# Kernel tuning notes

Measured on AMD Instinct MI355X. Metric: run time of the kernel, lower is better.

Reference implementation:

```python
import jax, jax.numpy as jnp
import numpy as np

B, N, C = 8, 2049, 768
H, NB = 12, 4
HD = C // H          # 64
SPB = (N - 1) // NB  # 512
SCALE = HD ** -0.5
EPS = 1e-6


def layer_norm(x, w, b):
    mu = jnp.mean(x, axis=-1, keepdims=True)
    var = jnp.mean((x - mu) ** 2, axis=-1, keepdims=True)
    return (x - mu) * jax.lax.rsqrt(var + EPS) * w + b


def setup_inputs() -> dict:
    key = jax.random.key(0)
    ks = jax.random.split(key, 6)
    s = lambda fan_in: 1.0 / np.sqrt(fan_in)
    return {
        "x": jax.random.normal(ks[0], (B, N, C), jnp.float32),
        "ln1_w": jnp.ones((C,), jnp.float32),
        "ln1_b": jnp.zeros((C,), jnp.float32),
        "qkv_w": jax.random.normal(ks[1], (3 * C, C), jnp.float32) * s(C),
        "proj_w": jax.random.normal(ks[2], (C, C), jnp.float32) * s(C),
        "proj_b": jnp.zeros((C,), jnp.float32),
        "ln2_w": jnp.ones((C,), jnp.float32),
        "ln2_b": jnp.zeros((C,), jnp.float32),
        "fc1_w": jax.random.normal(ks[3], (4 * C, C), jnp.float32) * s(C),
        "fc1_b": jnp.zeros((4 * C,), jnp.float32),
        "fc2_w": jax.random.normal(ks[4], (C, 4 * C), jnp.float32) * s(4 * C),
        "fc2_b": jnp.zeros((C,), jnp.float32),
    }


def _sdpa(q, k, v):
    # q:[...,Q,D] k,v:[...,K,D]
    scores = jnp.einsum("...qd,...kd->...qk", q, k) * SCALE
    return jnp.einsum("...qk,...kd->...qd", jax.nn.softmax(scores, axis=-1), v)


def _attention(h, qkv_w, proj_w, proj_b):
    # h: [B,N,C] (already layer-normed)
    qkv = (h @ qkv_w.T).reshape(B, N, 3, H, HD).transpose(2, 0, 3, 1, 4)  # [3,B,H,N,HD]
    q, k, v = qkv[0], qkv[1], qkv[2]

    # cls token attends globally over all N keys
    cls_att = _sdpa(q[:, :, 0:1, :], k, v)            # [B,H,1,HD]
    cls = cls_att.reshape(B, 1, C) + h[:, 0:1, :]      # benign reshape (seq=1)

    qkv_c = (cls @ qkv_w.T).reshape(B, 1, 3, H, HD).transpose(2, 0, 3, 1, 4)  # [3,B,H,1,HD]
    qc, kc, vc = qkv_c[0], qkv_c[1], qkv_c[2]

    # per-branch local attention with shared cls kv prepended
    def branch(t, tc):
        tb = t[:, :, 1:, :].reshape(B, H, NB, SPB, HD)
        tcb = jnp.broadcast_to(tc[:, :, None, :, :], (B, H, NB, 1, HD))
        return jnp.concatenate([tcb, tb], axis=3)      # [B,H,NB,SPB+1,HD]

    out = _sdpa(branch(q, qc), branch(k, kc), branch(v, vc))[:, :, :, 1:, :]  # [B,H,NB,SPB,HD]
    # faithful replication of the source's reshape((B, spb, C)) on a [B,H,spb,HD]
    # tensor WITHOUT head transpose (raw row-major reinterpretation):
    out = out.transpose(0, 2, 1, 3, 4).reshape(B, NB, SPB, C).reshape(B, NB * SPB, C)

    y = jnp.concatenate([cls, out], axis=1)            # [B,N,C]
    return y @ proj_w.T + proj_b


def reference(x, ln1_w, ln1_b, qkv_w, proj_w, proj_b, ln2_w, ln2_b, fc1_w, fc1_b, fc2_w, fc2_b):
    x = x + _attention(layer_norm(x, ln1_w, ln1_b), qkv_w, proj_w, proj_b)
    h = layer_norm(x, ln2_w, ln2_b)
    h = jax.nn.gelu(h @ fc1_w.T + fc1_b, approximate=False) @ fc2_w.T + fc2_b
    return x + h
```

## Files before the change

### kernel.cpp

```cpp
#include <hip/hip_runtime.h>
#include <hip/hip_bf16.h>

typedef unsigned short u16;
typedef __attribute__((ext_vector_type(8))) short s16x8;
typedef __attribute__((ext_vector_type(4))) float f32x4;

#define MFMA16 __builtin_amdgcn_mfma_f32_16x16x32_bf16
#define AS1 __attribute__((address_space(1)))
#define AS3 __attribute__((address_space(3)))

__device__ __forceinline__ u16 f2bf(float f) {
    union { __hip_bfloat16 h; u16 u; } cv;
    cv.h = __float2bfloat16(f);
    return cv.u;
}
__device__ __forceinline__ float bf2f(u16 u) {
    unsigned int v = ((unsigned int)u) << 16;
    return __uint_as_float(v);
}
__device__ __forceinline__ void gll16(const u16* g, u16* l) {
    __builtin_amdgcn_global_load_lds((AS1 void*)g, (AS3 void*)l, 16, 0, 0);
}

__global__ void cvt_kernel(const float* __restrict__ src, u16* __restrict__ dst, int n) {
    int i = (blockIdx.x * 256 + threadIdx.x) * 4;
    if (i + 3 < n) {
        float4 v = *(const float4*)&src[i];
        u16 o0 = f2bf(v.x), o1 = f2bf(v.y), o2 = f2bf(v.z), o3 = f2bf(v.w);
        ushort4 o; o.x = o0; o.y = o1; o.z = o2; o.w = o3;
        *(ushort4*)&dst[i] = o;
    }
}

__global__ __launch_bounds__(256) void ln_kernel(const float* __restrict__ x,
                                                 const float* __restrict__ w,
                                                 const float* __restrict__ b,
                                                 u16* __restrict__ out) {
    int tok = blockIdx.x;
    int tid = threadIdx.x;
    const float* xr = x + (size_t)tok * 768;
    float v0 = xr[tid], v1 = xr[tid + 256], v2 = xr[tid + 512];
    float s = v0 + v1 + v2;
    float s2 = v0 * v0 + v1 * v1 + v2 * v2;
    #pragma unroll
    for (int d = 1; d < 64; d <<= 1) { s += __shfl_xor(s, d); s2 += __shfl_xor(s2, d); }
    __shared__ float red[8];
    int wv = tid >> 6, l = tid & 63;
    if (l == 0) { red[wv] = s; red[4 + wv] = s2; }
    __syncthreads();
    s = red[0] + red[1] + red[2] + red[3];
    s2 = red[4] + red[5] + red[6] + red[7];
    float mu = s * (1.0f / 768.0f);
    float var = s2 * (1.0f / 768.0f) - mu * mu;
    float rs = rsqrtf(var + 1e-6f);
    u16* orow = out + (size_t)tok * 768;
    orow[tid]       = f2bf((v0 - mu) * rs * w[tid]       + b[tid]);
    orow[tid + 256] = f2bf((v1 - mu) * rs * w[tid + 256] + b[tid + 256]);
    orow[tid + 512] = f2bf((v2 - mu) * rs * w[tid + 512] + b[tid + 512]);
}

template<int EPI>
__global__ __launch_bounds__(256, 2) void gemm_bt(const u16* __restrict__ A,
                                                  const u16* __restrict__ Bw,
                                                  const float* __restrict__ bias,
                                                  const float* __restrict__ res,
                                                  float* __restrict__ outF,
                                                  u16* __restrict__ outU,
                                                  int M, int N, int K) {
    __shared__ u16 lds[8192];
    const int tid = threadIdx.x;
    const int l = tid & 63, w = tid >> 6;
    const int wm = w >> 1, wn = w & 1;
    const int g = l >> 4, c = l & 15;
    const int m0 = blockIdx.y * 128, n0 = blockIdx.x * 128;

    f32x4 zf = {0.f, 0.f, 0.f, 0.f};
    f32x4 acc[4][4];
    #pragma unroll
    for (int m = 0; m < 4; ++m)
        #pragma unroll
        for (int n = 0; n < 4; ++n) acc[m][n] = zf;

    const u16* aS[2]; const u16* bS[2];
    #pragma unroll
    for (int iss = 0; iss < 2; ++iss) {
        int fs = iss * 256 + tid;
        int r = fs >> 2;
        int gk = (fs & 3) ^ ((r >> 1) & 3);
        int ra = m0 + r; if (ra > M - 1) ra = M - 1;
        aS[iss] = A + (size_t)ra * K + gk * 8;
        bS[iss] = Bw + (size_t)(n0 + r) * K + gk * 8;
    }
    u16* aD0 = &lds[(0   + w * 64) * 8];
    u16* aD1 = &lds[(256 + w * 64) * 8];
    u16* bD0 = &lds[4096 + (0   + w * 64) * 8];
    u16* bD1 = &lds[4096 + (256 + w * 64) * 8];

    int aoff[4], boff[4];
    #pragma unroll
    for (int m = 0; m < 4; ++m) {
        int r = wm * 64 + m * 16 + c;
        aoff[m] = r * 32 + ((g ^ ((r >> 1) & 3)) * 8);
        int rb = wn * 64 + m * 16 + c;
        boff[m] = 4096 + rb * 32 + ((g ^ ((rb >> 1) & 3)) * 8);
    }

    for (int k0 = 0; k0 < K; k0 += 32) {
        gll16(aS[0] + k0, aD0);
        gll16(aS[1] + k0, aD1);
        gll16(bS[0] + k0, bD0);
        gll16(bS[1] + k0, bD1);
        __syncthreads();
        s16x8 af[4], bfr[4];
        #pragma unroll
        for (int m = 0; m < 4; ++m) af[m] = *(const s16x8*)&lds[aoff[m]];
        #pragma unroll
        for (int n = 0; n < 4; ++n) bfr[n] = *(const s16x8*)&lds[boff[n]];
        #pragma unroll
        for (int m = 0; m < 4; ++m)
            #pragma unroll
            for (int n = 0; n < 4; ++n)
                acc[m][n] = MFMA16(af[m], bfr[n], acc[m][n], 0, 0, 0);
        __syncthreads();
    }

    #pragma unroll
    for (int n = 0; n < 4; ++n) {
        int col = n0 + wn * 64 + n * 16 + c;
        float bv = (EPI >= 1) ? bias[col] : 0.0f;
        #pragma unroll
        for (int m = 0; m < 4; ++m) {
            int rowb = m0 + wm * 64 + m * 16 + g * 4;
            #pragma unroll
            for (int j = 0; j < 4; ++j) {
                int row = rowb + j;
                if (row < M) {
                    float v = acc[m][n][j];
                    size_t idx = (size_t)row * N + col;
                    if (EPI == 0) {
                        outU[idx] = f2bf(v);
                    } else if (EPI == 1) {
                        outF[idx] = res[idx] + v + bv;
                    } else {
                        float t = v + bv;
                        t = 0.5f * t * (1.0f + erff(t * 0.70710678118654752f));
                        outU[idx] = f2bf(t);
                    }
                }
            }
        }
    }
}

__global__ __launch_bounds__(256) void cls_part(const u16* __restrict__ qkv,
                                                float* __restrict__ part) {
    int bid = blockIdx.x;
    int ch = bid % 17;
    int hh = (bid / 17) % 12;
    int b = bid / (17 * 12);
    int tid = threadIdx.x, l = tid & 63, w = tid >> 6;
    size_t base = (size_t)b * 2049 * 2304;
    float qv = bf2f(qkv[base + hh * 64 + l]);
    __shared__ float sc[128];
    __shared__ float red[8];
    __shared__ float pv[4][64];
    int j0 = ch * 128;
    int nk = 2049 - j0; if (nk > 128) nk = 128;

    for (int jj = w; jj < nk; jj += 4) {
        float kv = bf2f(qkv[base + (size_t)(j0 + jj) * 2304 + 768 + hh * 64 + l]);
        float p = qv * kv;
        p += __shfl_xor(p, 1);  p += __shfl_xor(p, 2);  p += __shfl_xor(p, 4);
        p += __shfl_xor(p, 8);  p += __shfl_xor(p, 16); p += __shfl_xor(p, 32);
        if (l == 0) sc[jj] = p * 0.125f;
    }
    __syncthreads();
    float mx = -1e30f;
    for (int jj = tid; jj < nk; jj += 256) mx = fmaxf(mx, sc[jj]);
    #pragma unroll
    for (int d = 1; d < 64; d <<= 1) mx = fmaxf(mx, __shfl_xor(mx, d));
    if (l == 0) red[w] = mx;
    __syncthreads();
    mx = fmaxf(fmaxf(red[0], red[1]), fmaxf(red[2], red[3]));
    float sum = 0.0f;
    for (int jj = tid; jj < nk; jj += 256) {
        float p = __expf(sc[jj] - mx);
        sc[jj] = p;
        sum += p;
    }
    #pragma unroll
    for (int d = 1; d < 64; d <<= 1) sum += __shfl_xor(sum, d);
    if (l == 0) red[4 + w] = sum;
    __syncthreads();
    sum = red[4] + red[5] + red[6] + red[7];

    float acc = 0.0f;
    for (int jj = w; jj < nk; jj += 4)
        acc += sc[jj] * bf2f(qkv[base + (size_t)(j0 + jj) * 2304 + 1536 + hh * 64 + l]);
    pv[w][l] = acc;
    __syncthreads();
    if (tid < 64) {
        float o = pv[0][tid] + pv[1][tid] + pv[2][tid] + pv[3][tid];
        float* rec = part + ((size_t)(b * 12 + hh) * 17 + ch) * 66;
        rec[2 + tid] = o;
        if (tid == 0) { rec[0] = mx; rec[1] = sum; }
    }
}

__global__ __launch_bounds__(64) void cls_red(const float* __restrict__ part,
                                              const u16* __restrict__ h1,
                                              u16* __restrict__ y) {
    int bid = blockIdx.x;
    int hh = bid % 12, b = bid / 12;
    int l = threadIdx.x;
    const float* recs = part + (size_t)bid * 17 * 66;
    float M = -1e30f;
    #pragma unroll
    for (int i = 0; i < 17; ++i) M = fmaxf(M, recs[i * 66]);
    float den = 0.0f, o = 0.0f;
    #pragma unroll
    for (int i = 0; i < 17; ++i) {
        float scl = __expf(recs[i * 66] - M);
        den += scl * recs[i * 66 + 1];
        o += scl * recs[i * 66 + 2 + l];
    }
    o /= den;
    float r = bf2f(h1[(size_t)b * 2049 * 768 + hh * 64 + l]);
    y[(size_t)b * 1573632 + hh * 64 + l] = f2bf(o + r);
}

__global__ __launch_bounds__(256) void qkvc_gemm(const u16* __restrict__ y,
                                                 const u16* __restrict__ wq,
                                                 u16* __restrict__ qkvc) {
    int tid = threadIdx.x, l = tid & 63, w = tid >> 6;
    int oi = blockIdx.x * 4 + w;
    int b = oi / 2304, n = oi % 2304;
    float acc = 0.0f;
    #pragma unroll
    for (int i = 0; i < 12; ++i) {
        int k = i * 64 + l;
        acc += bf2f(y[(size_t)b * 1573632 + k]) * bf2f(wq[(size_t)n * 768 + k]);
    }
    #pragma unroll
    for (int d = 1; d < 64; d <<= 1) acc += __shfl_xor(acc, d);
    if (l == 0) qkvc[b * 2304 + n] = f2bf(acc);
}

__global__ __launch_bounds__(256, 2) void battn(const u16* __restrict__ qkv,
                                                const u16* __restrict__ qkvc,
                                                u16* __restrict__ y) {
    __shared__ u16 Vt[64 * 40];
    __shared__ u16 Pl[4][32 * 40];
    int bid = blockIdx.x;
    int quarter = bid & 3, nb = (bid >> 2) & 3, h = (bid >> 4) % 12, b = bid / 192;
    int tid = threadIdx.x, l = tid & 63, w = tid >> 6, g = l >> 4, c = l & 15;
    int qbase = quarter * 128 + w * 32;
    size_t tokbase = (size_t)b * 2049 + 1 + (size_t)nb * 512;

    s16x8 qf[2][2];
    #pragma unroll
    for (int qm = 0; qm < 2; ++qm)
        #pragma unroll
        for (int kc = 0; kc < 2; ++kc)
            qf[qm][kc] = *(const s16x8*)&qkv[(tokbase + qbase + qm * 16 + c) * 2304 + h * 64 + kc * 32 + g * 8];

    f32x4 zf = {0.f, 0.f, 0.f, 0.f};
    f32x4 o[2][4];
    float mst[2][4], lst[2][4];
    #pragma unroll
    for (int qm = 0; qm < 2; ++qm) {
        #pragma unroll
        for (int dn = 0; dn < 4; ++dn) o[qm][dn] = zf;
        #pragma unroll
        for (int j = 0; j < 4; ++j) { mst[qm][j] = -1e30f; lst[qm][j] = 0.0f; }
    }

    for (int t = 0; t <= 16; ++t) {
        __syncthreads();
        if (t < 16) {
            int key = tid & 31, dg = tid >> 5;
            s16x8 vv = *(const s16x8*)&qkv[(tokbase + t * 32 + key) * 2304 + 1536 + h * 64 + dg * 8];
            #pragma unroll
            for (int i = 0; i < 8; ++i) Vt[(dg * 8 + i) * 40 + key] = (u16)vv[i];
        } else {
            for (int i = tid; i < 2560; i += 256) Vt[i] = 0;
            __syncthreads();
            if (tid < 64) Vt[tid * 40] = qkvc[b * 2304 + 1536 + h * 64 + tid];
        }
        __syncthreads();

        f32x4 sfr[2][2];
        #pragma unroll
        for (int qm = 0; qm < 2; ++qm) { sfr[qm][0] = zf; sfr[qm][1] = zf; }

        if (t < 16) {
            #pragma unroll
            for (int kn = 0; kn < 2; ++kn)
                #pragma unroll
                for (int kc = 0; kc < 2; ++kc) {
                    s16x8 bk = *(const s16x8*)&qkv[(tokbase + t * 32 + kn * 16 + c) * 2304 + 768 + h * 64 + kc * 32 + g * 8];
                    #pragma unroll
                    for (int qm = 0; qm < 2; ++qm)
                        sfr[qm][kn] = MFMA16(qf[qm][kc], bk, sfr[qm][kn], 0, 0, 0);
                }
        } else {
            #pragma unroll
            for (int kc = 0; kc < 2; ++kc) {
                s16x8 bk = {0, 0, 0, 0, 0, 0, 0, 0};
                if (c == 0) bk = *(const s16x8*)&qkvc[b * 2304 + 768 + h * 64 + kc * 32 + g * 8];
                #pragma unroll
                for (int qm = 0; qm < 2; ++qm)
                    sfr[qm][0] = MFMA16(qf[qm][kc], bk, sfr[qm][0], 0, 0, 0);
            }
        }

        #pragma unroll
        for (int qm = 0; qm < 2; ++qm) {
            #pragma unroll
            for (int j = 0; j < 4; ++j) {
                float v0 = sfr[qm][0][j] * 0.125f;
                float v1 = (t < 16) ? sfr[qm][1][j] * 0.125f : -1e30f;
                if (t == 16 && c != 0) v0 = -1e30f;
                float tm = fmaxf(v0, v1);
                tm = fmaxf(tm, __shfl_xor(tm, 1));
                tm = fmaxf(tm, __shfl_xor(tm, 2));
                tm = fmaxf(tm, __shfl_xor(tm, 4));
                tm = fmaxf(tm, __shfl_xor(tm, 8));
                float mo = mst[qm][j];
                float mn = fmaxf(mo, tm);
                float scl = __expf(mo - mn);
                float p0 = __expf(v0 - mn);
                float p1 = __expf(v1 - mn);
                float ps = p0 + p1;
                ps += __shfl_xor(ps, 1); ps += __shfl_xor(ps, 2);
                ps += __shfl_xor(ps, 4); ps += __shfl_xor(ps, 8);
                lst[qm][j] = lst[qm][j] * scl + ps;
                mst[qm][j] = mn;
                #pragma unroll
                for (int dn = 0; dn < 4; ++dn) o[qm][dn][j] *= scl;
                int q = qm * 16 + g * 4 + j;
                Pl[w][q * 40 + c] = f2bf(p0);
                Pl[w][q * 40 + 16 + c] = f2bf(p1);
            }
        }

        s16x8 pa[2], vb[4];
        #pragma unroll
        for (int qm = 0; qm < 2; ++qm) pa[qm] = *(const s16x8*)&Pl[w][(qm * 16 + c) * 40 + g * 8];
        #pragma unroll
        for (int dn = 0; dn < 4; ++dn) vb[dn] = *(const s16x8*)&Vt[(dn * 16 + c) * 40 + g * 8];
        #pragma unroll
        for (int qm = 0; qm < 2; ++qm)
            #pragma unroll
            for (int dn = 0; dn < 4; ++dn)
                o[qm][dn] = MFMA16(pa[qm], vb[dn], o[qm][dn], 0, 0, 0);
    }

    size_t ybase = (size_t)b * 1573632 + 768 + (size_t)nb * 393216 + (size_t)h * 32768;
    #pragma unroll
    for (int qm = 0; qm < 2; ++qm)
        #pragma unroll
        for (int dn = 0; dn < 4; ++dn)
            #pragma unroll
            for (int j = 0; j < 4; ++j) {
                int q = qbase + qm * 16 + g * 4 + j;
                int d = dn * 16 + c;
                y[ybase + (size_t)q * 64 + d] = f2bf(o[qm][dn][j] / lst[qm][j]);
            }
}

extern "C" void kernel_launch(void* const* d_in, const int* in_sizes, int n_in,
                              void* d_out, int out_size, void* d_ws, size_t ws_size,
                              hipStream_t stream) {
    const float* x      = (const float*)d_in[0];
    const float* ln1_w  = (const float*)d_in[1];
    const float* ln1_b  = (const float*)d_in[2];
    const float* qkv_w  = (const float*)d_in[3];
    const float* proj_w = (const float*)d_in[4];
    const float* proj_b = (const float*)d_in[5];
    const float* ln2_w  = (const float*)d_in[6];
    const float* ln2_b  = (const float*)d_in[7];
    const float* fc1_w  = (const float*)d_in[8];
    const float* fc1_b  = (const float*)d_in[9];
    const float* fc2_w  = (const float*)d_in[10];
    const float* fc2_b  = (const float*)d_in[11];
    float* out = (float*)d_out;
    char* ws = (char*)d_ws;

    u16* Wq   = (u16*)(ws + 0);
    u16* Wp   = (u16*)(ws + 3538944);
    u16* Wf1  = (u16*)(ws + 4718592);
    u16* Wf2  = (u16*)(ws + 9437184);
    u16* h1   = (u16*)(ws + 14155776);
    u16* qkv  = (u16*)(ws + 39333888);
    u16* yb   = (u16*)(ws + 114868224);
    float* x2 = (float*)(ws + 140046336);
    u16* h2   = (u16*)(ws + 190402560);
    u16* qkvc = (u16*)(ws + 215580672);
    u16* gbuf = (u16*)(ws + 14155776);
    float* part = (float*)(ws + 140046336);

    cvt_kernel<<<1728, 256, 0, stream>>>(qkv_w, Wq, 1769472);
    cvt_kernel<<<576,  256, 0, stream>>>(proj_w, Wp, 589824);
    cvt_kernel<<<2304, 256, 0, stream>>>(fc1_w, Wf1, 2359296);
    cvt_kernel<<<2304, 256, 0, stream>>>(fc2_w, Wf2, 2359296);

    ln_kernel<<<16392, 256, 0, stream>>>(x, ln1_w, ln1_b, h1);
    gemm_bt<0><<<dim3(18, 129), 256, 0, stream>>>(h1, Wq, nullptr, nullptr, nullptr, qkv, 16392, 2304, 768);
    cls_part<<<1632, 256, 0, stream>>>(qkv, part);
    cls_red<<<96, 64, 0, stream>>>(part, h1, yb);
    qkvc_gemm<<<4608, 256, 0, stream>>>(yb, Wq, qkvc);
    battn<<<1536, 256, 0, stream>>>(qkv, qkvc, yb);
    gemm_bt<1><<<dim3(6, 129), 256, 0, stream>>>(yb, Wp, proj_b, x, x2, nullptr, 16392, 768, 768);
    ln_kernel<<<16392, 256, 0, stream>>>(x2, ln2_w, ln2_b, h2);
    gemm_bt<2><<<dim3(24, 129), 256, 0, stream>>>(h2, Wf1, fc1_b, nullptr, nullptr, gbuf, 16392, 3072, 768);
    gemm_bt<1><<<dim3(6, 129), 256, 0, stream>>>(gbuf, Wf2, fc2_b, x2, out, nullptr, 16392, 768, 3072);
}
```

Measured before the change: 788.2 us.

## Double-buffer LDS tiles in GEMM to overlap global loads with MFMA

Doubles the shared-memory buffer and restructures the K loop into a two-stage ping-pong pipeline. The next K tile is prefetched via global_load_lds while MFMAs consume the current one, hiding load latency behind compute and removing one barrier-then-wait per iteration. The larger LDS footprint can reduce occupancy. The loop also assumes K/32 is even.

Result: no change. 781.0 us (-0.9%).

```diff
diff --git a/kernel.cpp b/kernel.cpp
--- a/kernel.cpp
+++ b/kernel.cpp
@@ -67,7 +67,7 @@
                                                   float* __restrict__ outF,
                                                   u16* __restrict__ outU,
                                                   int M, int N, int K) {
-    __shared__ u16 lds[8192];
+    __shared__ u16 lds[16384];
     const int tid = threadIdx.x;
     const int l = tid & 63, w = tid >> 6;
     const int wm = w >> 1, wn = w & 1;
@@ -105,22 +105,56 @@
         boff[m] = 4096 + rb * 32 + ((g ^ ((rb >> 1) & 3)) * 8);
     }
 
-    for (int k0 = 0; k0 < K; k0 += 32) {
-        gll16(aS[0] + k0, aD0);
-        gll16(aS[1] + k0, aD1);
-        gll16(bS[0] + k0, bD0);
-        gll16(bS[1] + k0, bD1);
+    const int nt = K >> 5;
+
+    gll16(aS[0], aD0);
+    gll16(aS[1], aD1);
+    gll16(bS[0], bD0);
+    gll16(bS[1], bD1);
+    __syncthreads();
+
+    #pragma unroll 1
+    for (int t = 0; t < nt; t += 2) {
+        {
+            int k0 = (t + 1) << 5;
+            gll16(aS[0] + k0, aD0 + 8192);
+            gll16(aS[1] + k0, aD1 + 8192);
+            gll16(bS[0] + k0, bD0 + 8192);
+            gll16(bS[1] + k0, bD1 + 8192);
+        }
+        {
+            s16x8 af[4], bfr[4];
+            #pragma unroll
+            for (int m = 0; m < 4; ++m) af[m] = *(const s16x8*)&lds[aoff[m]];
+            #pragma unroll
+            for (int n = 0; n < 4; ++n) bfr[n] = *(const s16x8*)&lds[boff[n]];
+            #pragma unroll
+            for (int m = 0; m < 4; ++m)
+                #pragma unroll
+                for (int n = 0; n < 4; ++n)
+                    acc[m][n] = MFMA16(af[m], bfr[n], acc[m][n], 0, 0, 0);
+        }
         __syncthreads();
-        s16x8 af[4], bfr[4];
-        #pragma unroll
-        for (int m = 0; m < 4; ++m) af[m] = *(const s16x8*)&lds[aoff[m]];
-        #pragma unroll
-        for (int n = 0; n < 4; ++n) bfr[n] = *(const s16x8*)&lds[boff[n]];
-        #pragma unroll
-        for (int m = 0; m < 4; ++m)
-            #pragma unroll
-            for (int n = 0; n < 4; ++n)
-                acc[m][n] = MFMA16(af[m], bfr[n], acc[m][n], 0, 0, 0);
+
+        if (t + 2 < nt) {
+            int k0 = (t + 2) << 5;
+            gll16(aS[0] + k0, aD0);
+            gll16(aS[1] + k0, aD1);
+            gll16(bS[0] + k0, bD0);
+            gll16(bS[1] + k0, bD1);
+        }
+        {
+            s16x8 af[4], bfr[4];
+            #pragma unroll
+            for (int m = 0; m < 4; ++m) af[m] = *(const s16x8*)&lds[8192 + aoff[m]];
+            #pragma unroll
+            for (int n = 0; n < 4; ++n) bfr[n] = *(const s16x8*)&lds[8192 + boff[n]];
+            #pragma unroll
+            for (int m = 0; m < 4; ++m)
+                #pragma unroll
+                for (int n = 0; n < 4; ++n)
+                    acc[m][n] = MFMA16(af[m], bfr[n], acc[m][n], 0, 0, 0);
+        }
         __syncthreads();
     }
 
```

## Triple-buffer GEMM K-loop, remap blocks across XCDs, use tanh GELU

Applied to the files above, without the earlier changes.

The GEMM main loop moves from a single LDS buffer with two barriers per K-step to a three-stage ring. Async global-to-LDS loads for future tiles are issued while the current tile is computed, gated by s_waitcnt vmcnt plus a barrier. Workgroup IDs are remapped so consecutive tiles land on the same XCD, for better L2 reuse, and the exact erf GELU is replaced by an exp/rcp tanh-style approximation. The cost is triple the LDS footprint, an assumption that K/32 is a multiple of 3, and a small numerical deviation from exact GELU.

Measured after the change: 826.5 us. 4.9% more time.

```diff
diff --git a/kernel.cpp b/kernel.cpp
--- a/kernel.cpp
+++ b/kernel.cpp
@@ -67,12 +67,20 @@
                                                   float* __restrict__ outF,
                                                   u16* __restrict__ outU,
                                                   int M, int N, int K) {
-    __shared__ u16 lds[8192];
+    __shared__ u16 lds[24576];
     const int tid = threadIdx.x;
     const int l = tid & 63, w = tid >> 6;
     const int wm = w >> 1, wn = w & 1;
     const int g = l >> 4, c = l & 15;
-    const int m0 = blockIdx.y * 128, n0 = blockIdx.x * 128;
+
+    const int gx = gridDim.x, gyd = gridDim.y;
+    const int nwg = gx * gyd;
+    const int orig = blockIdx.y * gx + blockIdx.x;
+    const int q8 = nwg >> 3, r8 = nwg & 7;
+    const int xcd = orig & 7;
+    const int wgid = ((xcd < r8) ? xcd * (q8 + 1) : r8 * (q8 + 1) + (xcd - r8) * q8) + (orig >> 3);
+    const int m0 = (wgid % gyd) * 128;
+    const int n0 = (wgid / gyd) * 128;
 
     f32x4 zf = {0.f, 0.f, 0.f, 0.f};
     f32x4 acc[4][4];
@@ -91,10 +99,6 @@
         aS[iss] = A + (size_t)ra * K + gk * 8;
         bS[iss] = Bw + (size_t)(n0 + r) * K + gk * 8;
     }
-    u16* aD0 = &lds[(0   + w * 64) * 8];
-    u16* aD1 = &lds[(256 + w * 64) * 8];
-    u16* bD0 = &lds[4096 + (0   + w * 64) * 8];
-    u16* bD1 = &lds[4096 + (256 + w * 64) * 8];
 
     int aoff[4], boff[4];
     #pragma unroll
@@ -105,24 +109,49 @@
         boff[m] = 4096 + rb * 32 + ((g ^ ((rb >> 1) & 3)) * 8);
     }
 
-    for (int k0 = 0; k0 < K; k0 += 32) {
-        gll16(aS[0] + k0, aD0);
-        gll16(aS[1] + k0, aD1);
-        gll16(bS[0] + k0, bD0);
-        gll16(bS[1] + k0, bD1);
-        __syncthreads();
-        s16x8 af[4], bfr[4];
-        #pragma unroll
-        for (int m = 0; m < 4; ++m) af[m] = *(const s16x8*)&lds[aoff[m]];
-        #pragma unroll
-        for (int n = 0; n < 4; ++n) bfr[n] = *(const s16x8*)&lds[boff[n]];
-        #pragma unroll
-        for (int m = 0; m < 4; ++m)
-            #pragma unroll
-            for (int n = 0; n < 4; ++n)
-                acc[m][n] = MFMA16(af[m], bfr[n], acc[m][n], 0, 0, 0);
-        __syncthreads();
-    }
+#define STAGE(k, bb) { \
+        const int k0_ = (k) << 5; \
+        gll16(aS[0] + k0_, &lds[(bb) + w * 512]); \
+        gll16(aS[1] + k0_, &lds[(bb) + 2048 + w * 512]); \
+        gll16(bS[0] + k0_, &lds[(bb) + 4096 + w * 512]); \
+        gll16(bS[1] + k0_, &lds[(bb) + 6144 + w * 512]); \
+    }
+#define COMPUTE(bb) { \
+        s16x8 af[4], bfr[4]; \
+        _Pragma("unroll") \
+        for (int m = 0; m < 4; ++m) af[m] = *(const s16x8*)&lds[(bb) + aoff[m]]; \
+        _Pragma("unroll") \
+        for (int n = 0; n < 4; ++n) bfr[n] = *(const s16x8*)&lds[(bb) + boff[n]]; \
+        _Pragma("unroll") \
+        for (int m = 0; m < 4; ++m) \
+            _Pragma("unroll") \
+            for (int n = 0; n < 4; ++n) \
+                acc[m][n] = MFMA16(af[m], bfr[n], acc[m][n], 0, 0, 0); \
+    }
+#define WAITBAR4 asm volatile("s_waitcnt vmcnt(4)\n\ts_barrier" ::: "memory");
+#define WAITBAR0 asm volatile("s_waitcnt vmcnt(0)\n\ts_barrier" ::: "memory");
+
+    const int nt = K >> 5;
+
+    STAGE(0, 0);
+    STAGE(1, 8192);
+
+    int t = 0;
+    #pragma unroll 1
+    for (int it = 0; it < nt / 3 - 1; ++it) {
+        WAITBAR4; STAGE(t + 2, 16384); COMPUTE(0);
+        WAITBAR4; STAGE(t + 3, 0);     COMPUTE(8192);
+        WAITBAR4; STAGE(t + 4, 8192);  COMPUTE(16384);
+        t += 3;
+    }
+    WAITBAR4; STAGE(t + 2, 16384); COMPUTE(0);
+    WAITBAR4;                      COMPUTE(8192);
+    WAITBAR0;                      COMPUTE(16384);
+
+#undef STAGE
+#undef COMPUTE
+#undef WAITBAR4
+#undef WAITBAR0
 
     #pragma unroll
     for (int n = 0; n < 4; ++n) {
@@ -142,9 +171,10 @@
                     } else if (EPI == 1) {
                         outF[idx] = res[idx] + v + bv;
                     } else {
-                        float t = v + bv;
-                        t = 0.5f * t * (1.0f + erff(t * 0.70710678118654752f));
-                        outU[idx] = f2bf(t);
+                        float tt = v + bv;
+                        float sg = __expf(-(1.59576912f * tt + 0.0713548162f * tt * tt * tt));
+                        float rr = tt * __builtin_amdgcn_rcpf(1.0f + sg);
+                        outU[idx] = f2bf(rr);
                     }
                 }
             }
```

## Enlarge GEMM tiles to 256x256 with double-buffered LDS and tanh-form GELU

Applied to the files above, without the earlier changes.

The bf16 GEMM moves from 128x128 tiles with 256 threads to 256x256 tiles with 512 threads and a K-step of 64. LDS is double-buffered so the next tile's global-to-LDS loads are issued while the current tile is computed, which halves the barriers per K element and raises operand reuse. The fc1 epilogue replaces erf-based GELU with the sigmoid form of the tanh approximation (fast exp and reciprocal), trading a small accuracy deviation for cheaper math. The 128 KB of LDS and the larger accumulator set lower occupancy, and the bigger tiles cut grid parallelism, notably for the N=768 GEMMs, which now launch only 195 blocks.

Result: slower. 1.028 ms (+30.5%).

```diff
diff --git a/kernel.cpp b/kernel.cpp
--- a/kernel.cpp
+++ b/kernel.cpp
@@ -60,77 +60,96 @@
 }
 
 template<int EPI>
-__global__ __launch_bounds__(256, 2) void gemm_bt(const u16* __restrict__ A,
+__global__ __launch_bounds__(512, 2) void gemm_bt(const u16* __restrict__ A,
                                                   const u16* __restrict__ Bw,
                                                   const float* __restrict__ bias,
                                                   const float* __restrict__ res,
                                                   float* __restrict__ outF,
                                                   u16* __restrict__ outU,
                                                   int M, int N, int K) {
-    __shared__ u16 lds[8192];
+    __shared__ u16 lds[65536];
     const int tid = threadIdx.x;
     const int l = tid & 63, w = tid >> 6;
-    const int wm = w >> 1, wn = w & 1;
+    const int wr = w >> 2, wc = w & 3;
     const int g = l >> 4, c = l & 15;
-    const int m0 = blockIdx.y * 128, n0 = blockIdx.x * 128;
+    const int m0 = blockIdx.y * 256, n0 = blockIdx.x * 256;
 
     f32x4 zf = {0.f, 0.f, 0.f, 0.f};
-    f32x4 acc[4][4];
-    #pragma unroll
-    for (int m = 0; m < 4; ++m)
+    f32x4 acc[8][4];
+    #pragma unroll
+    for (int m = 0; m < 8; ++m)
         #pragma unroll
         for (int n = 0; n < 4; ++n) acc[m][n] = zf;
 
-    const u16* aS[2]; const u16* bS[2];
-    #pragma unroll
-    for (int iss = 0; iss < 2; ++iss) {
-        int fs = iss * 256 + tid;
-        int r = fs >> 2;
-        int gk = (fs & 3) ^ ((r >> 1) & 3);
+    const u16* aP[4]; const u16* bP[4]; int dOff[4];
+    #pragma unroll
+    for (int i = 0; i < 4; ++i) {
+        int fs = i * 512 + tid;
+        int r = fs >> 3;
+        int gk = (fs & 7) ^ ((r >> 1) & 7);
         int ra = m0 + r; if (ra > M - 1) ra = M - 1;
-        aS[iss] = A + (size_t)ra * K + gk * 8;
-        bS[iss] = Bw + (size_t)(n0 + r) * K + gk * 8;
-    }
-    u16* aD0 = &lds[(0   + w * 64) * 8];
-    u16* aD1 = &lds[(256 + w * 64) * 8];
-    u16* bD0 = &lds[4096 + (0   + w * 64) * 8];
-    u16* bD1 = &lds[4096 + (256 + w * 64) * 8];
-
-    int aoff[4], boff[4];
-    #pragma unroll
-    for (int m = 0; m < 4; ++m) {
-        int r = wm * 64 + m * 16 + c;
-        aoff[m] = r * 32 + ((g ^ ((r >> 1) & 3)) * 8);
-        int rb = wn * 64 + m * 16 + c;
-        boff[m] = 4096 + rb * 32 + ((g ^ ((rb >> 1) & 3)) * 8);
-    }
-
-    for (int k0 = 0; k0 < K; k0 += 32) {
-        gll16(aS[0] + k0, aD0);
-        gll16(aS[1] + k0, aD1);
-        gll16(bS[0] + k0, bD0);
-        gll16(bS[1] + k0, bD1);
+        aP[i] = A + (size_t)ra * K + gk * 8;
+        bP[i] = Bw + (size_t)(n0 + r) * K + gk * 8;
+        dOff[i] = fs * 8;
+    }
+
+    const int swz = (c >> 1) & 7;
+    int aRow[8], bRow[4], slotU[2];
+    #pragma unroll
+    for (int m = 0; m < 8; ++m) aRow[m] = (wr * 128 + m * 16 + c) * 64;
+    #pragma unroll
+    for (int n = 0; n < 4; ++n) bRow[n] = 16384 + (wc * 64 + n * 16 + c) * 64;
+    slotU[0] = ((0 + g) ^ swz) * 8;
+    slotU[1] = ((4 + g) ^ swz) * 8;
+
+#define STAGE(t, bb) { \
+        const int k0_ = (t) * 64; \
+        _Pragma("unroll") \
+        for (int i = 0; i < 4; ++i) gll16(aP[i] + k0_, &lds[(bb) + dOff[i]]); \
+        _Pragma("unroll") \
+        for (int i = 0; i < 4; ++i) gll16(bP[i] + k0_, &lds[(bb) + 16384 + dOff[i]]); \
+    }
+#define COMPUTE(bb) { \
+        _Pragma("unroll") \
+        for (int kk = 0; kk < 2; ++kk) { \
+            s16x8 af[8], bf[4]; \
+            _Pragma("unroll") \
+            for (int m = 0; m < 8; ++m) af[m] = *(const s16x8*)&lds[(bb) + aRow[m] + slotU[kk]]; \
+            _Pragma("unroll") \
+            for (int n = 0; n < 4; ++n) bf[n] = *(const s16x8*)&lds[(bb) + bRow[n] + slotU[kk]]; \
+            _Pragma("unroll") \
+            for (int m = 0; m < 8; ++m) \
+                _Pragma("unroll") \
+                for (int n = 0; n < 4; ++n) \
+                    acc[m][n] = MFMA16(af[m], bf[n], acc[m][n], 0, 0, 0); \
+        } \
+    }
+
+    const int nt = K >> 6;
+
+    STAGE(0, 0);
+    __syncthreads();
+
+    #pragma unroll 1
+    for (int t = 0; t < nt; t += 2) {
+        STAGE(t + 1, 32768);
+        COMPUTE(0);
         __syncthreads();
-        s16x8 af[4], bfr[4];
-        #pragma unroll
-        for (int m = 0; m < 4; ++m) af[m] = *(const s16x8*)&lds[aoff[m]];
-        #pragma unroll
-        for (int n = 0; n < 4; ++n) bfr[n] = *(const s16x8*)&lds[boff[n]];
-        #pragma unroll
-        for (int m = 0; m < 4; ++m)
-            #pragma unroll
-            for (int n = 0; n < 4; ++n)
-                acc[m][n] = MFMA16(af[m], bfr[n], acc[m][n], 0, 0, 0);
+        if (t + 2 < nt) STAGE(t + 2, 0);
+        COMPUTE(32768);
         __syncthreads();
     }
 
+#undef STAGE
+#undef COMPUTE
+
     #pragma unroll
     for (int n = 0; n < 4; ++n) {
-        int col = n0 + wn * 64 + n * 16 + c;
+        int col = n0 + wc * 64 + n * 16 + c;
         float bv = (EPI >= 1) ? bias[col] : 0.0f;
         #pragma unroll
-        for (int m = 0; m < 4; ++m) {
-            int rowb = m0 + wm * 64 + m * 16 + g * 4;
+        for (int m = 0; m < 8; ++m) {
+            int rowb = m0 + wr * 128 + m * 16 + g * 4;
             #pragma unroll
             for (int j = 0; j < 4; ++j) {
                 int row = rowb + j;
@@ -142,9 +161,10 @@
                     } else if (EPI == 1) {
                         outF[idx] = res[idx] + v + bv;
                     } else {
-                        float t = v + bv;
-                        t = 0.5f * t * (1.0f + erff(t * 0.70710678118654752f));
-                        outU[idx] = f2bf(t);
+                        float tt = v + bv;
+                        float sg = __expf(-(1.59576912f * tt + 0.0713548162f * tt * tt * tt));
+                        float rr = tt * __builtin_amdgcn_rcpf(1.0f + sg);
+                        outU[idx] = f2bf(rr);
                     }
                 }
             }
@@ -406,13 +426,13 @@
     cvt_kernel<<<2304, 256, 0, stream>>>(fc2_w, Wf2, 2359296);
 
     ln_kernel<<<16392, 256, 0, stream>>>(x, ln1_w, ln1_b, h1);
-    gemm_bt<0><<<dim3(18, 129), 256, 0, stream>>>(h1, Wq, nullptr, nullptr, nullptr, qkv, 16392, 2304, 768);
+    gemm_bt<0><<<dim3(9, 65), 512, 0, stream>>>(h1, Wq, nullptr, nullptr, nullptr, qkv, 16392, 2304, 768);
     cls_part<<<1632, 256, 0, stream>>>(qkv, part);
     cls_red<<<96, 64, 0, stream>>>(part, h1, yb);
     qkvc_gemm<<<4608, 256, 0, stream>>>(yb, Wq, qkvc);
     battn<<<1536, 256, 0, stream>>>(qkv, qkvc, yb);
-    gemm_bt<1><<<dim3(6, 129), 256, 0, stream>>>(yb, Wp, proj_b, x, x2, nullptr, 16392, 768, 768);
+    gemm_bt<1><<<dim3(3, 65), 512, 0, stream>>>(yb, Wp, proj_b, x, x2, nullptr, 16392, 768, 768);
     ln_kernel<<<16392, 256, 0, stream>>>(x2, ln2_w, ln2_b, h2);
-    gemm_bt<2><<<dim3(24, 129), 256, 0, stream>>>(h2, Wf1, fc1_b, nullptr, nullptr, gbuf, 16392, 3072, 768);
-    gemm_bt<1><<<dim3(6, 129), 256, 0, stream>>>(gbuf, Wf2, fc2_b, x2, out, nullptr, 16392, 768, 3072);
-}
+    gemm_bt<2><<<dim3(12, 65), 512, 0, stream>>>(h2, Wf1, fc1_b, nullptr, nullptr, gbuf, 16392, 3072, 768);
+    gemm_bt<1><<<dim3(3, 65), 512, 0, stream>>>(gbuf, Wf2, fc2_b, x2, out, nullptr, 16392, 768, 3072);
+}
```
